# Kernel optimization log

Measured on AMD Instinct MI355X. Metric: run time of the kernel, lower is better.

The kernel has to match this reference:

```python
import jax, jax.numpy as jnp
import numpy as np

N = 50000      # total nodes (batched graphs)
E = 800000     # edges per hop-set
B = 128        # number of graphs in batch
F_IN = 1024    # num_features_pro
D = 128        # hidden*16, heads=1


def setup_inputs() -> dict:
    key = jax.random.key(0)
    ks = jax.random.split(key, 32)
    s = 0.05
    def ei(k):
        return jax.random.randint(k, (2, E), 0, N, dtype=jnp.int32)
    inp = {
        'pro1_x': jax.random.normal(ks[0], (N, F_IN), jnp.float32),
        'pro1_ei1': ei(ks[1]), 'pro1_ei2': ei(ks[2]), 'pro1_ei3': ei(ks[3]),
        'pro1_batch': jnp.sort(jax.random.randint(ks[4], (N,), 0, B, dtype=jnp.int32)),
        'pro2_x': jax.random.normal(ks[5], (N, F_IN), jnp.float32),
        'pro2_ei1': ei(ks[6]), 'pro2_ei2': ei(ks[7]), 'pro2_ei3': ei(ks[8]),
        'pro2_batch': jnp.sort(jax.random.randint(ks[9], (N,), 0, B, dtype=jnp.int32)),
        # GATConv params (pro1_conv1 / pro2_conv1), shared across hop sets per branch
        'W1': jax.random.normal(ks[10], (F_IN, D), jnp.float32) * s,
        'a1_src': jax.random.normal(ks[11], (D,), jnp.float32) * s,
        'a1_dst': jax.random.normal(ks[12], (D,), jnp.float32) * s,
        'b1': jnp.zeros((D,), jnp.float32),
        'p1fc_W': jax.random.normal(ks[13], (D, D), jnp.float32) * s,
        'p1fc_b': jnp.zeros((D,), jnp.float32),
        'W2': jax.random.normal(ks[14], (F_IN, D), jnp.float32) * s,
        'a2_src': jax.random.normal(ks[15], (D,), jnp.float32) * s,
        'a2_dst': jax.random.normal(ks[16], (D,), jnp.float32) * s,
        'b2': jnp.zeros((D,), jnp.float32),
        'p2fc_W': jax.random.normal(ks[17], (D, D), jnp.float32) * s,
        'p2fc_b': jnp.zeros((D,), jnp.float32),
        'fc1_W': jax.random.normal(ks[18], (2 * D, 256), jnp.float32) * s,
        'fc1_b': jnp.zeros((256,), jnp.float32),
        'fc2_W': jax.random.normal(ks[19], (256, 64), jnp.float32) * s,
        'fc2_b': jnp.zeros((64,), jnp.float32),
        'out_W': jax.random.normal(ks[20], (64, 1), jnp.float32) * s,
        'out_b': jnp.zeros((1,), jnp.float32),
    }
    return inp


def _gat(x, ei, W, a_src, a_dst, b):
    # PyG GATConv, heads=1, add_self_loops=True, dropout off (eval)
    n = x.shape[0]
    h = x @ W                                   # [N, D]
    loops = jnp.arange(n, dtype=ei.dtype)
    src = jnp.concatenate([ei[0], loops])
    dst = jnp.concatenate([ei[1], loops])
    al_s = h @ a_src                            # [N]
    al_d = h @ a_dst
    e = jax.nn.leaky_relu(al_s[src] + al_d[dst], 0.2)   # per-edge logits
    m = jax.ops.segment_max(e, dst, num_segments=n)
    ex = jnp.exp(e - m[dst])
    denom = jax.ops.segment_sum(ex, dst, num_segments=n)
    alpha = ex / denom[dst]
    out = jax.ops.segment_sum(alpha[:, None] * h[src], dst, num_segments=n)
    return out + b


def _lrelu(v):
    return jax.nn.leaky_relu(v, 0.01)  # nn.LeakyReLU default slope


def _branch(x, e1, e2, e3, batch, W, a_s, a_d, b, fcW, fcb):
    h = _lrelu(_gat(x, e1, W, a_s, a_d, b))
    h = h + _lrelu(_gat(x, e2, W, a_s, a_d, b))
    h = h + _lrelu(_gat(x, e3, W, a_s, a_d, b))  # num_hops>=2 branch taken
    counts = jax.ops.segment_sum(jnp.ones((x.shape[0],), x.dtype), batch, num_segments=B)
    pooled = jax.ops.segment_sum(h, batch, num_segments=B) / jnp.maximum(counts, 1.0)[:, None]
    return _lrelu(pooled @ fcW + fcb)


def reference(pro1_x, pro1_ei1, pro1_ei2, pro1_ei3, pro1_batch,
              pro2_x, pro2_ei1, pro2_ei2, pro2_ei3, pro2_batch,
              W1, a1_src, a1_dst, b1, p1fc_W, p1fc_b,
              W2, a2_src, a2_dst, b2, p2fc_W, p2fc_b,
              fc1_W, fc1_b, fc2_W, fc2_b, out_W, out_b):
    x1 = _branch(pro1_x, pro1_ei1, pro1_ei2, pro1_ei3, pro1_batch, W1, a1_src, a1_dst, b1, p1fc_W, p1fc_b)
    x2 = _branch(pro2_x, pro2_ei1, pro2_ei2, pro2_ei3, pro2_batch, W2, a2_src, a2_dst, b2, p2fc_W, p2fc_b)
    xc = jnp.concatenate([x1, x2], axis=1)      # [B, 256]
    xc = _lrelu(xc @ fc1_W + fc1_b)
    xc = _lrelu(xc @ fc2_W + fc2_b)
    return jax.nn.sigmoid(xc @ out_W + out_b)   # [B, 1]
```

## Files before the change

kernel.cpp:

```cpp
#include <hip/hip_runtime.h>
#include <hip/hip_bf16.h>
#include <math.h>

#define N_NODES 50000
#define N_EDGES 800000
#define N_GRAPH 128
#define F_IN    1024
#define D_HID   128
#define NT3     (3*N_NODES)
#define LOG2E   1.44269504f

#define NPB_SH  9
#define NPB     512
#define NB      ((NT3 + NPB - 1) / NPB)
#define CAP     10240
#define EPB     4096
#define NBIN_PB ((3*N_EDGES + EPB - 1) / EPB)

typedef __bf16 bf16x8 __attribute__((ext_vector_type(8)));
typedef float  f32x4  __attribute__((ext_vector_type(4)));
typedef float  f32x2  __attribute__((ext_vector_type(2)));

__device__ __forceinline__ float lrelu01(float x){ return x > 0.f ? x : 0.01f*x; }
__device__ __forceinline__ float lrelu02(float x){ return x > 0.f ? x : 0.2f*x; }
__device__ __forceinline__ ushort f2bf(float v){
    __hip_bfloat16 hb = __float2bfloat16(v);
    return *reinterpret_cast<ushort*>(&hb);
}
__device__ __forceinline__ unsigned char f2fp8(float v){
    return (unsigned char)(__builtin_amdgcn_cvt_pk_fp8_f32(v, v, 0, false) & 0xFF);
}
__device__ __forceinline__ void fma8pk(uint2 u, f32x2 w2, f32x2* acc2){
    acc2[0] += w2 * __builtin_amdgcn_cvt_pk_f32_fp8(u.x, false);
    acc2[1] += w2 * __builtin_amdgcn_cvt_pk_f32_fp8(u.x, true);
    acc2[2] += w2 * __builtin_amdgcn_cvt_pk_f32_fp8(u.y, false);
    acc2[3] += w2 * __builtin_amdgcn_cvt_pk_f32_fp8(u.y, true);
}

__global__ void k_prep(const float* __restrict__ W0, const float* __restrict__ W1,
                       ushort* __restrict__ Wt, int* __restrict__ gcur){
    int b = blockIdx.x, t = threadIdx.x;
    if (b < 1024){
        int idx = b*256 + t;
        int br  = idx >> 17;
        int r   = idx & 131071;
        int n = r >> 10, k = r & 1023;
        const float* W = br ? W1 : W0;
        Wt[idx] = f2bf(W[k*D_HID + n]);
    } else {
        for (int i=t; i<2*NB; i+=256) gcur[i] = 0;
    }
}

#define BM  64
#define BK  64
#define LDP 72

__global__ __launch_bounds__(256) void k_gemm(const float* __restrict__ X0, const float* __restrict__ X1,
                                              const ushort* __restrict__ Wt,
                                              const float* __restrict__ as0, const float* __restrict__ ad0,
                                              const float* __restrict__ as1, const float* __restrict__ ad1,
                                              unsigned char* __restrict__ H8,
                                              float* __restrict__ als, float* __restrict__ ald){
    __shared__ ushort As[BM*LDP];
    __shared__ ushort Bs[D_HID*LDP];
    __shared__ float alp[4][2][64];
    int br = blockIdx.y;
    const float*  X   = br ? X1 : X0;
    const float*  asr = br ? as1 : as0;
    const float*  adr = br ? ad1 : ad0;
    const ushort* Wtb = Wt + (size_t)br*D_HID*F_IN;
    unsigned char* Hbb = H8 + (size_t)br*N_NODES*D_HID;

    int tid  = threadIdx.x;
    int m0   = blockIdx.x * BM;
    int lane = tid & 63;
    int wave = tid >> 6;
    int l15 = lane & 15, l4 = lane >> 4;
    int wcol = wave * 32;

    float4 pa[4];
    uint4  pb[4];

    auto loadA = [&](int kt){
        #pragma unroll
        for (int i=0;i<4;i++){
            int q = tid + i*256; int row = q >> 4; int kq = (q & 15) << 2;
            int gr = m0 + row;
            pa[i] = (gr < N_NODES) ? *reinterpret_cast<const float4*>(X + (size_t)gr*F_IN + kt + kq)
                                   : make_float4(0.f,0.f,0.f,0.f);
        }
    };
    auto loadB = [&](int kt){
        #pragma unroll
        for (int i=0;i<4;i++){
            int q = tid + i*256; int row = q >> 3; int ck = q & 7;
            pb[i] = *reinterpret_cast<const uint4*>(Wtb + row*F_IN + kt + ck*8);
        }
    };
    auto stage = [&](){
        #pragma unroll
        for (int i=0;i<4;i++){
            int q = tid + i*256; int row = q >> 4; int kq = (q & 15) << 2;
            ushort4 b; b.x=f2bf(pa[i].x); b.y=f2bf(pa[i].y); b.z=f2bf(pa[i].z); b.w=f2bf(pa[i].w);
            *reinterpret_cast<ushort4*>(&As[row*LDP + kq]) = b;
        }
        #pragma unroll
        for (int i=0;i<4;i++){
            int q = tid + i*256; int row = q >> 3; int ck = q & 7;
            *reinterpret_cast<uint2*>(&Bs[row*LDP + ck*8])     = make_uint2(pb[i].x, pb[i].y);
            *reinterpret_cast<uint2*>(&Bs[row*LDP + ck*8 + 4]) = make_uint2(pb[i].z, pb[i].w);
        }
    };

    f32x4 acc[4][2];
    #pragma unroll
    for (int i=0;i<4;i++) for (int j=0;j<2;j++) acc[i][j] = (f32x4){0.f,0.f,0.f,0.f};

    loadA(0); loadB(0);
    for (int kt = 0; kt < F_IN; kt += BK) {
        stage();
        __syncthreads();
        if (kt + BK < F_IN){ loadA(kt+BK); loadB(kt+BK); }
        #pragma unroll
        for (int kk = 0; kk < BK; kk += 32) {
            bf16x8 af[4], bfr[2];
            #pragma unroll
            for (int mi=0;mi<4;mi++)
                af[mi] = *reinterpret_cast<const bf16x8*>(&As[(mi*16+l15)*LDP + kk + l4*8]);
            #pragma unroll
            for (int ni=0;ni<2;ni++)
                bfr[ni] = *reinterpret_cast<const bf16x8*>(&Bs[(wcol+ni*16+l15)*LDP + kk + l4*8]);
            #pragma unroll
            for (int mi=0;mi<4;mi++)
                #pragma unroll
                for (int ni=0;ni<2;ni++)
                    acc[mi][ni] = __builtin_amdgcn_mfma_f32_16x16x32_bf16(af[mi], bfr[ni], acc[mi][ni], 0,0,0);
        }
        __syncthreads();
    }

    float asv[2], adv[2];
    #pragma unroll
    for (int ni=0;ni<2;ni++){
        int c = wcol + ni*16 + l15;
        asv[ni] = asr[c]; adv[ni] = adr[c];
    }
    #pragma unroll
    for (int mi=0;mi<4;mi++){
        #pragma unroll
        for (int jj=0;jj<4;jj++){
            int rrel = mi*16 + l4*4 + jj;
            int r = m0 + rrel;
            float ps = 0.f, pd = 0.f;
            #pragma unroll
            for (int ni=0;ni<2;ni++){
                float v = acc[mi][ni][jj];
                ps += v*asv[ni]; pd += v*adv[ni];
                if (r < N_NODES){
                    int c = wcol + ni*16 + l15;
                    Hbb[(size_t)r*D_HID + c] = f2fp8(v);
                }
            }
            #pragma unroll
            for (int o=1;o<16;o<<=1){ ps += __shfl_xor(ps,o); pd += __shfl_xor(pd,o); }
            if (l15 == 0){ alp[wave][0][rrel] = ps; alp[wave][1][rrel] = pd; }
        }
    }
    __syncthreads();
    if (tid < 64){
        int r = m0 + tid;
        if (r < N_NODES){
            float s_ = alp[0][0][tid]+alp[1][0][tid]+alp[2][0][tid]+alp[3][0][tid];
            float d_ = alp[0][1][tid]+alp[1][1][tid]+alp[2][1][tid]+alp[3][1][tid];
            als[br*N_NODES + r] = s_;
            ald[br*N_NODES + r] = d_;
        }
    }
}

__global__ __launch_bounds__(256) void k_bin(const int* __restrict__ e10, const int* __restrict__ e20,
                                             const int* __restrict__ e30,
                                             const int* __restrict__ e11, const int* __restrict__ e21,
                                             const int* __restrict__ e31,
                                             int* __restrict__ gcur, uint* __restrict__ pairs){
    __shared__ int hist[NB];
    __shared__ int start[NB];
    int blk = blockIdx.x;
    int br    = blk / NBIN_PB;
    int chunk = blk - br*NBIN_PB;
    int tid = threadIdx.x;
    for (int b=tid; b<NB; b+=256) hist[b]=0;
    __syncthreads();
    long base = (long)chunk * EPB;
    int  myb[16]; uint mypk[16];
    #pragma unroll
    for (int i=0;i<16;i++){
        long idx = base + i*256 + tid;
        int b = -1; uint pk = 0;
        if (idx < 3L*N_EDGES){
            int hop = (idx >= 2L*N_EDGES) ? 2 : (idx >= (long)N_EDGES) ? 1 : 0;
            int e   = (int)(idx - (long)hop*N_EDGES);
            const int* ei = (br==0) ? ((hop==0)?e10:(hop==1)?e20:e30)
                                    : ((hop==0)?e11:(hop==1)?e21:e31);
            int src = ei[e];
            int vd  = hop*N_NODES + ei[N_EDGES + e];
            b   = vd >> NPB_SH;
            pk  = (uint)src | ((uint)(vd & (NPB-1)) << 16);
            atomicAdd(&hist[b], 1);
        }
        myb[i]=b; mypk[i]=pk;
    }
    __syncthreads();
    for (int b=tid; b<NB; b+=256){
        int h = hist[b];
        start[b] = (h>0) ? atomicAdd(&gcur[br*NB + b], h) : 0;
    }
    __syncthreads();
    for (int b=tid; b<NB; b+=256) hist[b] = start[b];
    __syncthreads();
    #pragma unroll
    for (int i=0;i<16;i++){
        int b = myb[i];
        if (b >= 0){
            int pos = atomicAdd(&hist[b], 1);
            if (pos < CAP) pairs[((size_t)(br*NB + b))*CAP + pos] = mypk[i];
        }
    }
}

__global__ __launch_bounds__(256) void k_localcsr(const int* __restrict__ gcur,
                                                  const uint* __restrict__ pairs,
                                                  int* __restrict__ offs3, int* __restrict__ esrc){
    __shared__ int sc[512];
    __shared__ int deg[NPB];
    __shared__ int cur[NPB];
    __shared__ int ss[256];
    int gb = blockIdx.x;
    int br = gb / NB, bb = gb - br*NB;
    int t = threadIdx.x;
    sc[t]     = (t < NB)       ? min(gcur[br*NB + t], CAP) : 0;
    sc[t+256] = (t+256 < NB)   ? min(gcur[br*NB + t+256], CAP) : 0;
    __syncthreads();
    for (int o=1;o<512;o<<=1){
        int v0 = (t>=o)     ? sc[t-o]     : 0;
        int v1 = (t+256>=o) ? sc[t+256-o] : 0;
        __syncthreads();
        sc[t] += v0; sc[t+256] += v1;
        __syncthreads();
    }
    int base = (bb==0) ? 0 : sc[bb-1];
    int cnt  = sc[bb] - base;
    int* offsb = offs3 + (size_t)br*(NT3+1);
    if (bb == NB-1 && t == 0) offsb[NT3] = sc[NB-1];

    deg[t]=0; deg[t+256]=0;
    __syncthreads();
    const uint* pbuf = pairs + ((size_t)(br*NB + bb))*CAP;
    for (int i=t; i<cnt; i+=256) atomicAdd(&deg[pbuf[i] >> 16], 1);
    __syncthreads();
    int a0 = deg[2*t], a1 = deg[2*t+1];
    int ps = a0 + a1;
    ss[t] = ps; __syncthreads();
    for (int o=1;o<256;o<<=1){
        int u = (t>=o) ? ss[t-o] : 0;
        __syncthreads(); ss[t] += u; __syncthreads();
    }
    int ex = ss[t] - ps;
    __syncthreads();
    deg[2*t] = ex; deg[2*t+1] = ex + a0;
    cur[2*t] = ex; cur[2*t+1] = ex + a0;
    __syncthreads();
    int vd0 = bb << NPB_SH;
    for (int l=t; l<NPB; l+=256){
        int vd = vd0 + l;
        if (vd < NT3) offsb[vd] = base + deg[l];
    }
    int* esrcb = esrc + (size_t)br*3*N_EDGES;
    for (int i=t; i<cnt; i+=256){
        uint p = pbuf[i];
        int pos = atomicAdd(&cur[p >> 16], 1);
        esrcb[base + pos] = (int)(p & 0xFFFFu);
    }
}

__global__ __launch_bounds__(256) void k_gat3(const int* __restrict__ offs3, const int* __restrict__ esrc3,
                     const float* __restrict__ als, const float* __restrict__ ald,
                     const uint2* __restrict__ H8,
                     const float* __restrict__ bv0, const float* __restrict__ bv1,
                     float* __restrict__ hacc){
    __shared__ uint2 sh[4][64];
    int br = blockIdx.y;
    const int*   offs = offs3 + (size_t)br*(NT3+1);
    const int*   esrc = esrc3 + (size_t)br*3*N_EDGES;
    const float* alsb = als + br*N_NODES;
    const float* aldb = ald + br*N_NODES;
    const uint2* H8b  = H8 + (size_t)br*N_NODES*16;
    const float* bvec = br ? bv1 : bv0;
    float*       hb   = hacc + (size_t)br*N_NODES*D_HID;

    int lane = threadIdx.x & 63;
    int wl   = threadIdx.x >> 6;
    int d = blockIdx.x*4 + wl;
    if (d >= N_NODES) return;
    int g  = lane >> 4;
    int fl = lane & 15;
    float aldd  = aldb[d];
    float eself = lrelu02(alsb[d] + aldd);
    float exs   = __builtin_amdgcn_exp2f(eself * LOG2E);
    f32x2 self2[4];
    {
        uint2 hs = H8b[(size_t)d*16 + fl];
        f32x2 w2 = (f32x2){exs, exs};
        self2[0] = w2 * __builtin_amdgcn_cvt_pk_f32_fp8(hs.x, false);
        self2[1] = w2 * __builtin_amdgcn_cvt_pk_f32_fp8(hs.x, true);
        self2[2] = w2 * __builtin_amdgcn_cvt_pk_f32_fp8(hs.y, false);
        self2[3] = w2 * __builtin_amdgcn_cvt_pk_f32_fp8(hs.y, true);
    }
    f32x2 bv2[4];
    #pragma unroll
    for (int k=0;k<4;k++) bv2[k] = (f32x2){bvec[fl*8+2*k], bvec[fl*8+2*k+1]};
    f32x2 tot2[4];
    #pragma unroll
    for (int k=0;k<4;k++) tot2[k] = (f32x2){0.f, 0.f};

    for (int hop=0; hop<3; hop++){
        int s0 = offs[hop*N_NODES + d];
        int s1 = offs[hop*N_NODES + d + 1];
        int deg = s1 - s0;
        f32x2 acc2[4];
        #pragma unroll
        for (int k=0;k<4;k++) acc2[k] = (g==0) ? self2[k] : (f32x2){0.f,0.f};
        float es = 0.f;
        for (int base=0; base<deg; base+=64){
            int j = base + lane;
            int s = 0; float ex = 0.f;
            if (j < deg){
                s = esrc[s0 + j];
                ex = __builtin_amdgcn_exp2f(lrelu02(alsb[s] + aldd) * LOG2E);
            }
            es += ex;
            sh[wl][lane] = make_uint2((uint)s, __float_as_uint(ex));
            int cnt = min(64, deg - base);
            int i = g;
            for (; i + 4 < cnt; i += 8){
                uint2 seA = sh[wl][i];
                uint2 seB = sh[wl][i+4];
                uint2 hvA = H8b[(size_t)seA.x*16 + fl];
                uint2 hvB = H8b[(size_t)seB.x*16 + fl];
                float wA = __uint_as_float(seA.y);
                float wB = __uint_as_float(seB.y);
                fma8pk(hvA, (f32x2){wA,wA}, acc2);
                fma8pk(hvB, (f32x2){wB,wB}, acc2);
            }
            if (i < cnt){
                uint2 se = sh[wl][i];
                uint2 hv = H8b[(size_t)se.x*16 + fl];
                float w = __uint_as_float(se.y);
                fma8pk(hv, (f32x2){w,w}, acc2);
            }
        }
        for (int o=32;o;o>>=1) es += __shfl_xor(es,o);
        #pragma unroll
        for (int k=0;k<4;k++){
            float x0 = acc2[k][0], x1 = acc2[k][1];
            x0 += __shfl_xor(x0, 16); x0 += __shfl_xor(x0, 32);
            x1 += __shfl_xor(x1, 16); x1 += __shfl_xor(x1, 32);
            acc2[k][0] = x0; acc2[k][1] = x1;
        }
        float inv = 1.f / (es + exs);
        #pragma unroll
        for (int k=0;k<4;k++){
            tot2[k][0] += lrelu01(acc2[k][0]*inv + bv2[k][0]);
            tot2[k][1] += lrelu01(acc2[k][1]*inv + bv2[k][1]);
        }
    }
    if (g == 0){
        float4 w0 = make_float4(tot2[0][0],tot2[0][1],tot2[1][0],tot2[1][1]);
        float4 w1 = make_float4(tot2[2][0],tot2[2][1],tot2[3][0],tot2[3][1]);
        *reinterpret_cast<float4*>(hb + (size_t)d*D_HID + fl*8)     = w0;
        *reinterpret_cast<float4*>(hb + (size_t)d*D_HID + fl*8 + 4) = w1;
    }
}

__global__ __launch_bounds__(256) void k_pool_fc(const float* __restrict__ hacc,
                    const int* __restrict__ b0, const int* __restrict__ b1,
                    const float* __restrict__ pW0, const float* __restrict__ pb0,
                    const float* __restrict__ pW1, const float* __restrict__ pb1,
                    float* __restrict__ xb){
    __shared__ float sums[2][128];
    __shared__ float pl[128];
    int br = blockIdx.y;
    const float* hb   = hacc + (size_t)br*N_NODES*D_HID;
    const int*   batch= br ? b1 : b0;
    const float* fcW  = br ? pW1 : pW0;
    const float* fcb  = br ? pb1 : pb0;
    int g = blockIdx.x;
    int t = threadIdx.x;
    int lo=0, hi=N_NODES;
    while (lo<hi){ int mid=(lo+hi)>>1; if (batch[mid] < g) lo=mid+1; else hi=mid; }
    int s = lo;
    lo = s; hi = N_NODES;
    while (lo<hi){ int mid=(lo+hi)>>1; if (batch[mid] < g+1) lo=mid+1; else hi=mid; }
    int e = lo;
    int f = t & 127, half = t >> 7;
    float sum = 0.f;
    for (int n=s+half; n<e; n+=2) sum += hb[(size_t)n*D_HID + f];
    sums[half][f] = sum;
    __syncthreads();
    if (t < 128){
        float cnt = (float)(e - s);
        pl[t] = (sums[0][t] + sums[1][t]) / fmaxf(cnt, 1.0f);
    }
    __syncthreads();
    if (t < 128){
        float a = fcb[t];
        for (int k=0;k<128;k++) a += pl[k]*fcW[k*128 + t];
        xb[(br*N_GRAPH + g)*128 + t] = lrelu01(a);
    }
}

__global__ __launch_bounds__(256) void k_final(const float* __restrict__ xb,
                      const float* __restrict__ fc1W, const float* __restrict__ fc1b,
                      const float* __restrict__ fc2W, const float* __restrict__ fc2b,
                      const float* __restrict__ outW, const float* __restrict__ outb,
                      float* __restrict__ out){
    __shared__ float xc[256], y1[256], y2[64];
    int g = blockIdx.x, t = threadIdx.x;
    xc[t] = (t < 128) ? xb[g*128 + t] : xb[(N_GRAPH + g)*128 + (t-128)];
    __syncthreads();
    float a = fc1b[t];
    for (int k=0;k<256;k++) a += xc[k]*fc1W[k*256 + t];
    y1[t] = lrelu01(a);
    __syncthreads();
    if (t < 64){
        float a2 = fc2b[t];
        for (int k=0;k<256;k++) a2 += y1[k]*fc2W[k*64 + t];
        y2[t] = lrelu01(a2);
    }
    __syncthreads();
    if (t == 0){
        float z = outb[0];
        for (int k=0;k<64;k++) z += y2[k]*outW[k];
        out[g] = 1.f/(1.f + expf(-z));
    }
}

extern "C" void kernel_launch(void* const* d_in, const int* in_sizes, int n_in,
                              void* d_out, int out_size, void* d_ws, size_t ws_size,
                              hipStream_t stream){
    const float* X0 = (const float*)d_in[0];
    const float* X1 = (const float*)d_in[5];
    const int *e10=(const int*)d_in[1], *e20=(const int*)d_in[2], *e30=(const int*)d_in[3];
    const int *e11=(const int*)d_in[6], *e21=(const int*)d_in[7], *e31=(const int*)d_in[8];
    const int *b0=(const int*)d_in[4], *b1=(const int*)d_in[9];
    const float *W0=(const float*)d_in[10], *W1=(const float*)d_in[16];
    const float *as0=(const float*)d_in[11], *ad0=(const float*)d_in[12];
    const float *as1=(const float*)d_in[17], *ad1=(const float*)d_in[18];
    const float *bv0=(const float*)d_in[13], *bv1=(const float*)d_in[19];
    const float *pW0=(const float*)d_in[14], *pb0=(const float*)d_in[15];
    const float *pW1=(const float*)d_in[20], *pb1=(const float*)d_in[21];
    const float *fc1W=(const float*)d_in[22], *fc1b=(const float*)d_in[23];
    const float *fc2W=(const float*)d_in[24], *fc2b=(const float*)d_in[25];
    const float *outW=(const float*)d_in[26], *outb=(const float*)d_in[27];
    float* out = (float*)d_out;

    char* ws = (char*)d_ws;
    size_t o = 0;
    auto alloc = [&](size_t bytes)->char*{ char* p = ws + o; o += (bytes + 511) & ~(size_t)511; return p; };
    unsigned char* H8 = (unsigned char*)alloc((size_t)2*N_NODES*D_HID);
    float*  hacc  = (float*) alloc((size_t)2*N_NODES*D_HID*4);
    float*  als   = (float*) alloc((size_t)2*N_NODES*4);
    float*  ald   = (float*) alloc((size_t)2*N_NODES*4);
    int*    offs3 = (int*)   alloc((size_t)2*(NT3+1)*4);
    int*    esrc3 = (int*)   alloc((size_t)2*3*N_EDGES*4);
    int*    gcur  = (int*)   alloc((size_t)2*NB*4);
    uint*   pairs = (uint*)  alloc((size_t)2*NB*CAP*4);
    ushort* Wt    = (ushort*)alloc((size_t)2*D_HID*F_IN*2);
    float*  xb    = (float*) alloc((size_t)2*N_GRAPH*D_HID*4);

    k_prep    <<<1025, 256, 0, stream>>>(W0, W1, Wt, gcur);
    k_gemm    <<<dim3((N_NODES+BM-1)/BM, 2), 256, 0, stream>>>(X0, X1, Wt, as0, ad0, as1, ad1, H8, als, ald);
    k_bin     <<<2*NBIN_PB, 256, 0, stream>>>(e10, e20, e30, e11, e21, e31, gcur, pairs);
    k_localcsr<<<2*NB, 256, 0, stream>>>(gcur, pairs, offs3, esrc3);
    k_gat3    <<<dim3((N_NODES+3)/4, 2), 256, 0, stream>>>(offs3, esrc3, als, ald, (const uint2*)H8, bv0, bv1, hacc);
    k_pool_fc <<<dim3(N_GRAPH, 2), 256, 0, stream>>>(hacc, b0, b1, pW0, pb0, pW1, pb1, xb);
    k_final   <<<N_GRAPH, 256, 0, stream>>>(xb, fc1W, fc1b, fc2W, fc2b, outW, outb, out);
}
```

Baseline: 423.7 us.

## Use async global-to-LDS loads with XOR-swizzled double buffering in GEMM

Replaces the register-staged GEMM mainloop with direct global_load_lds transfers into double-buffered, XOR-swizzled shared memory. The fp32 X tile now stays fp32 in LDS and is converted to bf16 at fragment-read time. The aim is to remove register staging and per-thread conversion stores, and to overlap loading the next K tile with MFMA work. In exchange the K tile shrinks to 32, so there are twice as many iterations and barriers, and LDS traffic for A doubles because it is held as fp32. The only synchronisation is one __syncthreads per iteration, with no explicit wait on the async loads (vmcnt), so correctness depends on the barrier ordering those loads.

```diff
diff --git a/kernel.cpp b/kernel.cpp
--- a/kernel.cpp
+++ b/kernel.cpp
@@ -20,6 +20,7 @@
 typedef __bf16 bf16x8 __attribute__((ext_vector_type(8)));
 typedef float  f32x4  __attribute__((ext_vector_type(4)));
 typedef float  f32x2  __attribute__((ext_vector_type(2)));
+typedef ushort u16x8  __attribute__((ext_vector_type(8)));
 
 __device__ __forceinline__ float lrelu01(float x){ return x > 0.f ? x : 0.01f*x; }
 __device__ __forceinline__ float lrelu02(float x){ return x > 0.f ? x : 0.2f*x; }
@@ -29,6 +30,16 @@
 }
 __device__ __forceinline__ unsigned char f2fp8(float v){
     return (unsigned char)(__builtin_amdgcn_cvt_pk_fp8_f32(v, v, 0, false) & 0xFF);
+}
+__device__ __forceinline__ bf16x8 cvt8(float4 a, float4 b){
+    u16x8 u;
+    u[0]=f2bf(a.x); u[1]=f2bf(a.y); u[2]=f2bf(a.z); u[3]=f2bf(a.w);
+    u[4]=f2bf(b.x); u[5]=f2bf(b.y); u[6]=f2bf(b.z); u[7]=f2bf(b.w);
+    return *reinterpret_cast<bf16x8*>(&u);
+}
+__device__ __forceinline__ void gload16(const void* g, void* l){
+    __builtin_amdgcn_global_load_lds((const __attribute__((address_space(1))) unsigned int*)g,
+                                     (__attribute__((address_space(3))) unsigned int*)l, 16, 0, 0);
 }
 __device__ __forceinline__ void fma8pk(uint2 u, f32x2 w2, f32x2* acc2){
     acc2[0] += w2 * __builtin_amdgcn_cvt_pk_f32_fp8(u.x, false);
@@ -52,9 +63,8 @@
     }
 }
 
-#define BM  64
-#define BK  64
-#define LDP 72
+#define BM   64
+#define BKG  32
 
 __global__ __launch_bounds__(256) void k_gemm(const float* __restrict__ X0, const float* __restrict__ X1,
                                               const ushort* __restrict__ Wt,
@@ -62,8 +72,8 @@
                                               const float* __restrict__ as1, const float* __restrict__ ad1,
                                               unsigned char* __restrict__ H8,
                                               float* __restrict__ als, float* __restrict__ ald){
-    __shared__ ushort As[BM*LDP];
-    __shared__ ushort Bs[D_HID*LDP];
+    __shared__ __align__(16) float  Asl[2][2048];
+    __shared__ __align__(16) ushort Bsl[2][4096];
     __shared__ float alp[4][2][64];
     int br = blockIdx.y;
     const float*  X   = br ? X1 : X0;
@@ -79,64 +89,54 @@
     int l15 = lane & 15, l4 = lane >> 4;
     int wcol = wave * 32;
 
-    float4 pa[4];
-    uint4  pb[4];
-
-    auto loadA = [&](int kt){
-        #pragma unroll
-        for (int i=0;i<4;i++){
-            int q = tid + i*256; int row = q >> 4; int kq = (q & 15) << 2;
-            int gr = m0 + row;
-            pa[i] = (gr < N_NODES) ? *reinterpret_cast<const float4*>(X + (size_t)gr*F_IN + kt + kq)
-                                   : make_float4(0.f,0.f,0.f,0.f);
+    auto issue = [&](int kt, int buf){
+        #pragma unroll
+        for (int j=0;j<2;j++){
+            int o = wave*2048 + j*1024 + lane*16;
+            int row = o >> 7, chunk = (o >> 4) & 7;
+            int grow = min(m0 + row, N_NODES-1);
+            const float* g = X + (size_t)grow*F_IN + kt + ((chunk ^ (row & 7)) << 2);
+            gload16(g, (char*)&Asl[buf][0] + wave*2048 + j*1024);
+        }
+        #pragma unroll
+        for (int j=0;j<2;j++){
+            int o = wave*2048 + j*1024 + lane*16;
+            int row = o >> 6, chunk = (o >> 4) & 3;
+            const ushort* g = Wtb + (size_t)row*F_IN + kt + ((chunk ^ ((row >> 1) & 3)) << 3);
+            gload16(g, (char*)&Bsl[buf][0] + wave*2048 + j*1024);
         }
     };
-    auto loadB = [&](int kt){
-        #pragma unroll
-        for (int i=0;i<4;i++){
-            int q = tid + i*256; int row = q >> 3; int ck = q & 7;
-            pb[i] = *reinterpret_cast<const uint4*>(Wtb + row*F_IN + kt + ck*8);
-        }
-    };
-    auto stage = [&](){
-        #pragma unroll
-        for (int i=0;i<4;i++){
-            int q = tid + i*256; int row = q >> 4; int kq = (q & 15) << 2;
-            ushort4 b; b.x=f2bf(pa[i].x); b.y=f2bf(pa[i].y); b.z=f2bf(pa[i].z); b.w=f2bf(pa[i].w);
-            *reinterpret_cast<ushort4*>(&As[row*LDP + kq]) = b;
-        }
-        #pragma unroll
-        for (int i=0;i<4;i++){
-            int q = tid + i*256; int row = q >> 3; int ck = q & 7;
-            *reinterpret_cast<uint2*>(&Bs[row*LDP + ck*8])     = make_uint2(pb[i].x, pb[i].y);
-            *reinterpret_cast<uint2*>(&Bs[row*LDP + ck*8 + 4]) = make_uint2(pb[i].z, pb[i].w);
-        }
-    };
 
     f32x4 acc[4][2];
     #pragma unroll
     for (int i=0;i<4;i++) for (int j=0;j<2;j++) acc[i][j] = (f32x4){0.f,0.f,0.f,0.f};
 
-    loadA(0); loadB(0);
-    for (int kt = 0; kt < F_IN; kt += BK) {
-        stage();
-        __syncthreads();
-        if (kt + BK < F_IN){ loadA(kt+BK); loadB(kt+BK); }
-        #pragma unroll
-        for (int kk = 0; kk < BK; kk += 32) {
-            bf16x8 af[4], bfr[2];
-            #pragma unroll
-            for (int mi=0;mi<4;mi++)
-                af[mi] = *reinterpret_cast<const bf16x8*>(&As[(mi*16+l15)*LDP + kk + l4*8]);
+    issue(0, 0);
+    __syncthreads();
+
+    const int NT = F_IN / BKG;
+    for (int t = 0; t < NT; ++t){
+        int cur = t & 1;
+        if (t + 1 < NT) issue((t+1)*BKG, cur ^ 1);
+        bf16x8 af[4], bfr[2];
+        #pragma unroll
+        for (int mi=0;mi<4;mi++){
+            int row = mi*16 + l15;
+            const char* base = (const char*)&Asl[cur][0] + row*128;
+            float4 a0 = *(const float4*)(base + ((( 2*l4   ) ^ (row & 7)) << 4));
+            float4 a1 = *(const float4*)(base + (((2*l4 + 1) ^ (row & 7)) << 4));
+            af[mi] = cvt8(a0, a1);
+        }
+        #pragma unroll
+        for (int ni=0;ni<2;ni++){
+            int row = wcol + ni*16 + l15;
+            bfr[ni] = *(const bf16x8*)((const char*)&Bsl[cur][0] + row*64 + ((l4 ^ ((l15 >> 1) & 3)) << 4));
+        }
+        #pragma unroll
+        for (int mi=0;mi<4;mi++)
             #pragma unroll
             for (int ni=0;ni<2;ni++)
-                bfr[ni] = *reinterpret_cast<const bf16x8*>(&Bs[(wcol+ni*16+l15)*LDP + kk + l4*8]);
-            #pragma unroll
-            for (int mi=0;mi<4;mi++)
-                #pragma unroll
-                for (int ni=0;ni<2;ni++)
-                    acc[mi][ni] = __builtin_amdgcn_mfma_f32_16x16x32_bf16(af[mi], bfr[ni], acc[mi][ni], 0,0,0);
-        }
+                acc[mi][ni] = __builtin_amdgcn_mfma_f32_16x16x32_bf16(af[mi], bfr[ni], acc[mi][ni], 0,0,0);
         __syncthreads();
     }
 
```

Result: slower. 436.3 us (+3.0%).

## Merge GEMM and edge binning into one interleaved kernel launch

Applied to the files above, without the earlier changes.

Fuses the node-feature GEMM and the edge-binning pass into a single kernel. The first blocks alternate between GEMM and binning work, and the leftover GEMM blocks follow, so the memory-bound binning overlaps the MFMA-bound GEMM on the same CUs. The gcur counter zeroing moves from the prep kernel to hipMemsetAsync. The cost is shared LDS sized for the GEMM and higher register pressure from the merged kernel, which may lower occupancy for the binning blocks.

```diff
diff --git a/kernel.cpp b/kernel.cpp
--- a/kernel.cpp
+++ b/kernel.cpp
@@ -17,6 +17,14 @@
 #define EPB     4096
 #define NBIN_PB ((3*N_EDGES + EPB - 1) / EPB)
 
+#define BM  64
+#define BK  64
+#define LDP 72
+#define MBLK      ((N_NODES + BM - 1) / BM)
+#define GEMM_BLKS (2*MBLK)
+#define BIN_BLKS  (2*NBIN_PB)
+#define SMEM_BYTES (BM*LDP*2 + D_HID*LDP*2 + 4*2*64*4)
+
 typedef __bf16 bf16x8 __attribute__((ext_vector_type(8)));
 typedef float  f32x4  __attribute__((ext_vector_type(4)));
 typedef float  f32x2  __attribute__((ext_vector_type(2)));
@@ -38,193 +46,191 @@
 }
 
 __global__ void k_prep(const float* __restrict__ W0, const float* __restrict__ W1,
-                       ushort* __restrict__ Wt, int* __restrict__ gcur){
-    int b = blockIdx.x, t = threadIdx.x;
-    if (b < 1024){
-        int idx = b*256 + t;
-        int br  = idx >> 17;
-        int r   = idx & 131071;
-        int n = r >> 10, k = r & 1023;
-        const float* W = br ? W1 : W0;
-        Wt[idx] = f2bf(W[k*D_HID + n]);
-    } else {
-        for (int i=t; i<2*NB; i+=256) gcur[i] = 0;
-    }
-}
-
-#define BM  64
-#define BK  64
-#define LDP 72
-
-__global__ __launch_bounds__(256) void k_gemm(const float* __restrict__ X0, const float* __restrict__ X1,
-                                              const ushort* __restrict__ Wt,
-                                              const float* __restrict__ as0, const float* __restrict__ ad0,
-                                              const float* __restrict__ as1, const float* __restrict__ ad1,
-                                              unsigned char* __restrict__ H8,
-                                              float* __restrict__ als, float* __restrict__ ald){
-    __shared__ ushort As[BM*LDP];
-    __shared__ ushort Bs[D_HID*LDP];
-    __shared__ float alp[4][2][64];
-    int br = blockIdx.y;
-    const float*  X   = br ? X1 : X0;
-    const float*  asr = br ? as1 : as0;
-    const float*  adr = br ? ad1 : ad0;
-    const ushort* Wtb = Wt + (size_t)br*D_HID*F_IN;
-    unsigned char* Hbb = H8 + (size_t)br*N_NODES*D_HID;
-
-    int tid  = threadIdx.x;
-    int m0   = blockIdx.x * BM;
-    int lane = tid & 63;
-    int wave = tid >> 6;
-    int l15 = lane & 15, l4 = lane >> 4;
-    int wcol = wave * 32;
-
-    float4 pa[4];
-    uint4  pb[4];
-
-    auto loadA = [&](int kt){
-        #pragma unroll
-        for (int i=0;i<4;i++){
-            int q = tid + i*256; int row = q >> 4; int kq = (q & 15) << 2;
-            int gr = m0 + row;
-            pa[i] = (gr < N_NODES) ? *reinterpret_cast<const float4*>(X + (size_t)gr*F_IN + kt + kq)
-                                   : make_float4(0.f,0.f,0.f,0.f);
-        }
-    };
-    auto loadB = [&](int kt){
-        #pragma unroll
-        for (int i=0;i<4;i++){
-            int q = tid + i*256; int row = q >> 3; int ck = q & 7;
-            pb[i] = *reinterpret_cast<const uint4*>(Wtb + row*F_IN + kt + ck*8);
-        }
-    };
-    auto stage = [&](){
-        #pragma unroll
-        for (int i=0;i<4;i++){
-            int q = tid + i*256; int row = q >> 4; int kq = (q & 15) << 2;
-            ushort4 b; b.x=f2bf(pa[i].x); b.y=f2bf(pa[i].y); b.z=f2bf(pa[i].z); b.w=f2bf(pa[i].w);
-            *reinterpret_cast<ushort4*>(&As[row*LDP + kq]) = b;
-        }
-        #pragma unroll
-        for (int i=0;i<4;i++){
-            int q = tid + i*256; int row = q >> 3; int ck = q & 7;
-            *reinterpret_cast<uint2*>(&Bs[row*LDP + ck*8])     = make_uint2(pb[i].x, pb[i].y);
-            *reinterpret_cast<uint2*>(&Bs[row*LDP + ck*8 + 4]) = make_uint2(pb[i].z, pb[i].w);
-        }
-    };
-
-    f32x4 acc[4][2];
-    #pragma unroll
-    for (int i=0;i<4;i++) for (int j=0;j<2;j++) acc[i][j] = (f32x4){0.f,0.f,0.f,0.f};
-
-    loadA(0); loadB(0);
-    for (int kt = 0; kt < F_IN; kt += BK) {
-        stage();
-        __syncthreads();
-        if (kt + BK < F_IN){ loadA(kt+BK); loadB(kt+BK); }
-        #pragma unroll
-        for (int kk = 0; kk < BK; kk += 32) {
-            bf16x8 af[4], bfr[2];
-            #pragma unroll
-            for (int mi=0;mi<4;mi++)
-                af[mi] = *reinterpret_cast<const bf16x8*>(&As[(mi*16+l15)*LDP + kk + l4*8]);
-            #pragma unroll
-            for (int ni=0;ni<2;ni++)
-                bfr[ni] = *reinterpret_cast<const bf16x8*>(&Bs[(wcol+ni*16+l15)*LDP + kk + l4*8]);
-            #pragma unroll
-            for (int mi=0;mi<4;mi++)
-                #pragma unroll
-                for (int ni=0;ni<2;ni++)
-                    acc[mi][ni] = __builtin_amdgcn_mfma_f32_16x16x32_bf16(af[mi], bfr[ni], acc[mi][ni], 0,0,0);
-        }
-        __syncthreads();
-    }
-
-    float asv[2], adv[2];
-    #pragma unroll
-    for (int ni=0;ni<2;ni++){
-        int c = wcol + ni*16 + l15;
-        asv[ni] = asr[c]; adv[ni] = adr[c];
-    }
-    #pragma unroll
-    for (int mi=0;mi<4;mi++){
-        #pragma unroll
-        for (int jj=0;jj<4;jj++){
-            int rrel = mi*16 + l4*4 + jj;
-            int r = m0 + rrel;
-            float ps = 0.f, pd = 0.f;
-            #pragma unroll
-            for (int ni=0;ni<2;ni++){
-                float v = acc[mi][ni][jj];
-                ps += v*asv[ni]; pd += v*adv[ni];
-                if (r < N_NODES){
-                    int c = wcol + ni*16 + l15;
-                    Hbb[(size_t)r*D_HID + c] = f2fp8(v);
-                }
-            }
-            #pragma unroll
-            for (int o=1;o<16;o<<=1){ ps += __shfl_xor(ps,o); pd += __shfl_xor(pd,o); }
-            if (l15 == 0){ alp[wave][0][rrel] = ps; alp[wave][1][rrel] = pd; }
-        }
-    }
-    __syncthreads();
-    if (tid < 64){
-        int r = m0 + tid;
-        if (r < N_NODES){
-            float s_ = alp[0][0][tid]+alp[1][0][tid]+alp[2][0][tid]+alp[3][0][tid];
-            float d_ = alp[0][1][tid]+alp[1][1][tid]+alp[2][1][tid]+alp[3][1][tid];
-            als[br*N_NODES + r] = s_;
-            ald[br*N_NODES + r] = d_;
-        }
-    }
-}
-
-__global__ __launch_bounds__(256) void k_bin(const int* __restrict__ e10, const int* __restrict__ e20,
+                       ushort* __restrict__ Wt){
+    int idx = blockIdx.x*256 + threadIdx.x;
+    int br  = idx >> 17;
+    int r   = idx & 131071;
+    int n = r >> 10, k = r & 1023;
+    const float* W = br ? W1 : W0;
+    Wt[idx] = f2bf(W[k*D_HID + n]);
+}
+
+__global__ __launch_bounds__(256) void k_fat(const float* __restrict__ X0, const float* __restrict__ X1,
+                                             const ushort* __restrict__ Wt,
+                                             const float* __restrict__ as0, const float* __restrict__ ad0,
+                                             const float* __restrict__ as1, const float* __restrict__ ad1,
+                                             unsigned char* __restrict__ H8,
+                                             float* __restrict__ als, float* __restrict__ ald,
+                                             const int* __restrict__ e10, const int* __restrict__ e20,
                                              const int* __restrict__ e30,
                                              const int* __restrict__ e11, const int* __restrict__ e21,
                                              const int* __restrict__ e31,
                                              int* __restrict__ gcur, uint* __restrict__ pairs){
-    __shared__ int hist[NB];
-    __shared__ int start[NB];
-    int blk = blockIdx.x;
-    int br    = blk / NBIN_PB;
-    int chunk = blk - br*NBIN_PB;
+    __shared__ __align__(16) char smem[SMEM_BYTES];
     int tid = threadIdx.x;
-    for (int b=tid; b<NB; b+=256) hist[b]=0;
-    __syncthreads();
-    long base = (long)chunk * EPB;
-    int  myb[16]; uint mypk[16];
-    #pragma unroll
-    for (int i=0;i<16;i++){
-        long idx = base + i*256 + tid;
-        int b = -1; uint pk = 0;
-        if (idx < 3L*N_EDGES){
-            int hop = (idx >= 2L*N_EDGES) ? 2 : (idx >= (long)N_EDGES) ? 1 : 0;
-            int e   = (int)(idx - (long)hop*N_EDGES);
-            const int* ei = (br==0) ? ((hop==0)?e10:(hop==1)?e20:e30)
-                                    : ((hop==0)?e11:(hop==1)?e21:e31);
-            int src = ei[e];
-            int vd  = hop*N_NODES + ei[N_EDGES + e];
-            b   = vd >> NPB_SH;
-            pk  = (uint)src | ((uint)(vd & (NPB-1)) << 16);
-            atomicAdd(&hist[b], 1);
-        }
-        myb[i]=b; mypk[i]=pk;
-    }
-    __syncthreads();
-    for (int b=tid; b<NB; b+=256){
-        int h = hist[b];
-        start[b] = (h>0) ? atomicAdd(&gcur[br*NB + b], h) : 0;
-    }
-    __syncthreads();
-    for (int b=tid; b<NB; b+=256) hist[b] = start[b];
-    __syncthreads();
-    #pragma unroll
-    for (int i=0;i<16;i++){
-        int b = myb[i];
-        if (b >= 0){
-            int pos = atomicAdd(&hist[b], 1);
-            if (pos < CAP) pairs[((size_t)(br*NB + b))*CAP + pos] = mypk[i];
+    int bid = blockIdx.x;
+    int is_bin, wid;
+    if (bid < 2*BIN_BLKS){ is_bin = bid & 1; wid = bid >> 1; }
+    else                 { is_bin = 0; wid = BIN_BLKS + (bid - 2*BIN_BLKS); }
+
+    if (!is_bin){
+        int br = wid / MBLK;
+        int mb = wid - br*MBLK;
+        ushort* As = (ushort*)smem;
+        ushort* Bs = (ushort*)(smem + BM*LDP*2);
+        float (*alp)[2][64] = (float(*)[2][64])(smem + BM*LDP*2 + D_HID*LDP*2);
+
+        const float*  X   = br ? X1 : X0;
+        const float*  asr = br ? as1 : as0;
+        const float*  adr = br ? ad1 : ad0;
+        const ushort* Wtb = Wt + (size_t)br*D_HID*F_IN;
+        unsigned char* Hbb = H8 + (size_t)br*N_NODES*D_HID;
+
+        int m0   = mb * BM;
+        int lane = tid & 63;
+        int wave = tid >> 6;
+        int l15 = lane & 15, l4 = lane >> 4;
+        int wcol = wave * 32;
+
+        float4 pa[4];
+        uint4  pb[4];
+
+        auto loadA = [&](int kt){
+            #pragma unroll
+            for (int i=0;i<4;i++){
+                int q = tid + i*256; int row = q >> 4; int kq = (q & 15) << 2;
+                int gr = m0 + row;
+                pa[i] = (gr < N_NODES) ? *reinterpret_cast<const float4*>(X + (size_t)gr*F_IN + kt + kq)
+                                       : make_float4(0.f,0.f,0.f,0.f);
+            }
+        };
+        auto loadB = [&](int kt){
+            #pragma unroll
+            for (int i=0;i<4;i++){
+                int q = tid + i*256; int row = q >> 3; int ck = q & 7;
+                pb[i] = *reinterpret_cast<const uint4*>(Wtb + row*F_IN + kt + ck*8);
+            }
+        };
+        auto stage = [&](){
+            #pragma unroll
+            for (int i=0;i<4;i++){
+                int q = tid + i*256; int row = q >> 4; int kq = (q & 15) << 2;
+                ushort4 b; b.x=f2bf(pa[i].x); b.y=f2bf(pa[i].y); b.z=f2bf(pa[i].z); b.w=f2bf(pa[i].w);
+                *reinterpret_cast<ushort4*>(&As[row*LDP + kq]) = b;
+            }
+            #pragma unroll
+            for (int i=0;i<4;i++){
+                int q = tid + i*256; int row = q >> 3; int ck = q & 7;
+                *reinterpret_cast<uint2*>(&Bs[row*LDP + ck*8])     = make_uint2(pb[i].x, pb[i].y);
+                *reinterpret_cast<uint2*>(&Bs[row*LDP + ck*8 + 4]) = make_uint2(pb[i].z, pb[i].w);
+            }
+        };
+
+        f32x4 acc[4][2];
+        #pragma unroll
+        for (int i=0;i<4;i++) for (int j=0;j<2;j++) acc[i][j] = (f32x4){0.f,0.f,0.f,0.f};
+
+        loadA(0); loadB(0);
+        for (int kt = 0; kt < F_IN; kt += BK) {
+            stage();
+            __syncthreads();
+            if (kt + BK < F_IN){ loadA(kt+BK); loadB(kt+BK); }
+            #pragma unroll
+            for (int kk = 0; kk < BK; kk += 32) {
+                bf16x8 af[4], bfr[2];
+                #pragma unroll
+                for (int mi=0;mi<4;mi++)
+                    af[mi] = *reinterpret_cast<const bf16x8*>(&As[(mi*16+l15)*LDP + kk + l4*8]);
+                #pragma unroll
+                for (int ni=0;ni<2;ni++)
+                    bfr[ni] = *reinterpret_cast<const bf16x8*>(&Bs[(wcol+ni*16+l15)*LDP + kk + l4*8]);
+                #pragma unroll
+                for (int mi=0;mi<4;mi++)
+                    #pragma unroll
+                    for (int ni=0;ni<2;ni++)
+                        acc[mi][ni] = __builtin_amdgcn_mfma_f32_16x16x32_bf16(af[mi], bfr[ni], acc[mi][ni], 0,0,0);
+            }
+            __syncthreads();
+        }
+
+        float asv[2], adv[2];
+        #pragma unroll
+        for (int ni=0;ni<2;ni++){
+            int c = wcol + ni*16 + l15;
+            asv[ni] = asr[c]; adv[ni] = adr[c];
+        }
+        #pragma unroll
+        for (int mi=0;mi<4;mi++){
+            #pragma unroll
+            for (int jj=0;jj<4;jj++){
+                int rrel = mi*16 + l4*4 + jj;
+                int r = m0 + rrel;
+                float ps = 0.f, pd = 0.f;
+                #pragma unroll
+                for (int ni=0;ni<2;ni++){
+                    float v = acc[mi][ni][jj];
+                    ps += v*asv[ni]; pd += v*adv[ni];
+                    if (r < N_NODES){
+                        int c = wcol + ni*16 + l15;
+                        Hbb[(size_t)r*D_HID + c] = f2fp8(v);
+                    }
+                }
+                #pragma unroll
+                for (int o=1;o<16;o<<=1){ ps += __shfl_xor(ps,o); pd += __shfl_xor(pd,o); }
+                if (l15 == 0){ alp[wave][0][rrel] = ps; alp[wave][1][rrel] = pd; }
+            }
+        }
+        __syncthreads();
+        if (tid < 64){
+            int r = m0 + tid;
+            if (r < N_NODES){
+                float s_ = alp[0][0][tid]+alp[1][0][tid]+alp[2][0][tid]+alp[3][0][tid];
+                float d_ = alp[0][1][tid]+alp[1][1][tid]+alp[2][1][tid]+alp[3][1][tid];
+                als[br*N_NODES + r] = s_;
+                ald[br*N_NODES + r] = d_;
+            }
+        }
+    } else {
+        int br    = wid / NBIN_PB;
+        int chunk = wid - br*NBIN_PB;
+        int* hist  = (int*)smem;
+        int* start = hist + NB;
+        for (int b=tid; b<NB; b+=256) hist[b]=0;
+        __syncthreads();
+        long base = (long)chunk * EPB;
+        int  myb[16]; uint mypk[16];
+        #pragma unroll
+        for (int i=0;i<16;i++){
+            long idx = base + i*256 + tid;
+            int b = -1; uint pk = 0;
+            if (idx < 3L*N_EDGES){
+                int hop = (idx >= 2L*N_EDGES) ? 2 : (idx >= (long)N_EDGES) ? 1 : 0;
+                int e   = (int)(idx - (long)hop*N_EDGES);
+                const int* ei = (br==0) ? ((hop==0)?e10:(hop==1)?e20:e30)
+                                        : ((hop==0)?e11:(hop==1)?e21:e31);
+                int src = ei[e];
+                int vd  = hop*N_NODES + ei[N_EDGES + e];
+                b   = vd >> NPB_SH;
+                pk  = (uint)src | ((uint)(vd & (NPB-1)) << 16);
+                atomicAdd(&hist[b], 1);
+            }
+            myb[i]=b; mypk[i]=pk;
+        }
+        __syncthreads();
+        for (int b=tid; b<NB; b+=256){
+            int h = hist[b];
+            start[b] = (h>0) ? atomicAdd(&gcur[br*NB + b], h) : 0;
+        }
+        __syncthreads();
+        for (int b=tid; b<NB; b+=256) hist[b] = start[b];
+        __syncthreads();
+        #pragma unroll
+        for (int i=0;i<16;i++){
+            int b = myb[i];
+            if (b >= 0){
+                int pos = atomicAdd(&hist[b], 1);
+                if (pos < CAP) pairs[((size_t)(br*NB + b))*CAP + pos] = mypk[i];
+            }
         }
     }
 }
@@ -479,9 +485,10 @@
     ushort* Wt    = (ushort*)alloc((size_t)2*D_HID*F_IN*2);
     float*  xb    = (float*) alloc((size_t)2*N_GRAPH*D_HID*4);
 
-    k_prep    <<<1025, 256, 0, stream>>>(W0, W1, Wt, gcur);
-    k_gemm    <<<dim3((N_NODES+BM-1)/BM, 2), 256, 0, stream>>>(X0, X1, Wt, as0, ad0, as1, ad1, H8, als, ald);
-    k_bin     <<<2*NBIN_PB, 256, 0, stream>>>(e10, e20, e30, e11, e21, e31, gcur, pairs);
+    hipMemsetAsync(gcur, 0, (size_t)2*NB*4, stream);
+    k_prep    <<<1024, 256, 0, stream>>>(W0, W1, Wt);
+    k_fat     <<<GEMM_BLKS + BIN_BLKS, 256, 0, stream>>>(X0, X1, Wt, as0, ad0, as1, ad1, H8, als, ald,
+                                                         e10, e20, e30, e11, e21, e31, gcur, pairs);
     k_localcsr<<<2*NB, 256, 0, stream>>>(gcur, pairs, offs3, esrc3);
     k_gat3    <<<dim3((N_NODES+3)/4, 2), 256, 0, stream>>>(offs3, esrc3, als, ald, (const uint2*)H8, bv0, bv1, hacc);
     k_pool_fc <<<dim3(N_GRAPH, 2), 256, 0, stream>>>(hacc, b0, b1, pW0, pb0, pW1, pb1, xb);
```

Measured after the change: 450.7 us. 6.4% more time.
